# Optimization experiments

Hardware: AMD Instinct MI355X
Metric: run time of the kernel (lower is better)

The kernel has to match this reference:

```python
import jax, jax.numpy as jnp
import numpy as np


def setup_inputs() -> dict:
    key = jax.random.key(0)
    k = jax.random.split(key, 6)
    B, S, d, n = 4, 4096, 1024, 64
    x = jax.random.normal(k[0], (B, S, d), dtype=jnp.float32)
    gate_W = jax.random.normal(k[1], (d, n), dtype=jnp.float32) / np.sqrt(d).astype(np.float32)
    gate_b = jnp.full((n,), 3.0, dtype=jnp.float32)  # nn.init.constant_(gate_proj.bias, 3.0)
    B_W = jax.random.normal(k[2], (d, n), dtype=jnp.float32) / np.sqrt(d).astype(np.float32)
    C_W = jax.random.normal(k[3], (n, d), dtype=jnp.float32) / np.sqrt(n).astype(np.float32)
    out_W = jax.random.normal(k[4], (d, d), dtype=jnp.float32) / np.sqrt(d).astype(np.float32)
    mix_weight = jnp.eye(n, dtype=jnp.float32) + 0.01 * jax.random.normal(k[5], (n, n), dtype=jnp.float32)
    return {"x": x, "gate_W": gate_W, "gate_b": gate_b, "B_W": B_W,
            "C_W": C_W, "out_W": out_W, "mix_weight": mix_weight, "chunk_size": 16}


def _ssm_forward(x, gate_W, gate_b, B_W, C_W, out_W, mix_weight, chunk_size):
    Bb, S, d = x.shape
    n = gate_W.shape[1]
    C = chunk_size
    K = S // C  # seq_len chosen divisible by chunk_size -> F.pad path is a no-op
    # Vectorized per-timestep projections (done once for the whole sequence)
    gates = jax.nn.sigmoid(jnp.einsum('bsd,dn->bsn', x, gate_W) + gate_b)  # a_t in (0,1)
    b_all = jnp.einsum('bsd,dn->bsn', x, B_W)
    a_ch = gates.reshape(Bb, K, C, n).transpose(1, 2, 0, 3)  # (K, C, B, n)
    b_ch = b_all.reshape(Bb, K, C, n).transpose(1, 2, 0, 3)

    def chunk_step(h_prev, ab):
        a_c, b_c = ab  # each (C, B, n)
        def step(h, t):
            a_t, b_t = t
            h = a_t * h + b_t
            return h, h
        h_final, h_stack = jax.lax.scan(step, h_prev, (a_c, b_c))  # h_stack: (C, B, n)
        gate_prod = jnp.prod(a_c, axis=0)  # (B, n) cumulative diag gates
        # T_chunk = mix @ diag(gate_prod): T[b,i,j] = mix[i,j] * gate_prod[b,j]
        T = mix_weight[None, :, :] * gate_prod[:, None, :]
        Th = jnp.einsum('bij,bj->bi', T, h_prev)
        b_chunk = h_final - Th
        h_next = Th + b_chunk  # canonical inter-chunk propagation: T @ h_prev + b_chunk
        return h_next, h_stack

    h0 = jnp.zeros((Bb, n), dtype=x.dtype)
    _, h_all = jax.lax.scan(chunk_step, h0, (a_ch, b_ch))  # (K, C, B, n)
    h_seq = h_all.transpose(2, 0, 1, 3).reshape(Bb, S, n)
    y = jnp.einsum('bsn,nd->bsd', h_seq, C_W)
    out_gate = jax.nn.sigmoid(jnp.einsum('bsd,de->bse', x, out_W))
    return y * out_gate


def reference(x, gate_W, gate_b, B_W, C_W, out_W, mix_weight, chunk_size):
    return _ssm_forward(x, gate_W, gate_b, B_W, C_W, out_W, mix_weight, chunk_size)
```

## Files before the change

kernel.cpp:

```cpp
#include <hip/hip_runtime.h>
#include <stdint.h>

typedef __attribute__((ext_vector_type(8))) short short8;
typedef __attribute__((ext_vector_type(4))) float f32x4;
typedef __attribute__((ext_vector_type(4))) float f4;
typedef __attribute__((ext_vector_type(4))) unsigned short us4;

typedef unsigned short ushort_t;

__device__ __forceinline__ ushort_t f2bf(float f) {
    union { float f; uint32_t u; } c; c.f = f;
    uint32_t u = c.u;
    uint32_t r = u + 0x7fffu + ((u >> 16) & 1u);
    return (ushort_t)(r >> 16);
}
__device__ __forceinline__ float bf2f(ushort_t h) {
    union { uint32_t u; float f; } c; c.u = ((uint32_t)h) << 16;
    return c.f;
}

typedef const __attribute__((address_space(1))) unsigned int as1_uint;
typedef __attribute__((address_space(3))) unsigned int as3_uint;
__device__ __forceinline__ void gload_lds16(const void* g, void* l) {
    __builtin_amdgcn_global_load_lds((as1_uint*)g, (as3_uint*)l, 16, 0, 0);
}

#define SWIDX(r, c) ((r) * 64 + ((c) ^ (((r) & 7) << 3)))

__global__ void prep_weights(const float* __restrict__ gate_W, const float* __restrict__ B_W,
                             const float* __restrict__ C_W, const float* __restrict__ out_W,
                             ushort_t* __restrict__ W1t_hi, ushort_t* __restrict__ W1t_lo,
                             ushort_t* __restrict__ outWt, ushort_t* __restrict__ Ct)
{
    int idx = blockIdx.x * 256 + threadIdx.x;
    int stride = gridDim.x * 256;
    for (int i = idx; i < 1024 * 1024; i += stride) {
        int nn = i >> 10, kk = i & 1023;
        outWt[i] = f2bf(out_W[kk * 1024 + nn]);
    }
    for (int i = idx; i < 128 * 1024; i += stride) {
        int nn = i >> 10, kk = i & 1023;
        float v = (nn < 64) ? gate_W[kk * 64 + nn] : B_W[kk * 64 + (nn - 64)];
        ushort_t h = f2bf(v);
        W1t_hi[i] = h;
        W1t_lo[i] = f2bf(v - bf2f(h));
    }
    for (int i = idx; i < 1024 * 64; i += stride) {
        int nn = i >> 6, kk = i & 63;
        Ct[i] = f2bf(C_W[kk * 1024 + nn]);
    }
}

__global__ __launch_bounds__(256, 2)
void p1_kernel(const float* __restrict__ x,
               const ushort_t* __restrict__ W1t_hi, const ushort_t* __restrict__ W1t_lo,
               ushort_t* __restrict__ x_hi, float* __restrict__ Zpart)
{
    __shared__ ushort_t Ash[128 * 64];
    __shared__ ushort_t Asl[128 * 64];
    __shared__ ushort_t Bsh[64 * 64];

    const int tid = threadIdx.x;
    const int wave = tid >> 6, lane = tid & 63;
    const int wm = wave >> 1, wn = wave & 1;
    const int s0 = blockIdx.x * 64;
    const int kc = blockIdx.y;

    f32x4 acc[4][2];
#pragma unroll
    for (int i = 0; i < 4; i++)
#pragma unroll
        for (int j = 0; j < 2; j++) { f32x4 z = {0.f,0.f,0.f,0.f}; acc[i][j] = z; }

    for (int kt = 0; kt < 8; ++kt) {
        const int k0 = kc * 512 + kt * 64;
#pragma unroll
        for (int p = 0; p < 4; ++p) {
            int c = p * 256 + wave * 64 + lane;
            int row = c >> 3, col = (c & 7) * 8;
            gload_lds16(W1t_hi + (size_t)row * 1024 + k0 + col,
                        &Ash[(p * 256 + wave * 64) * 8]);
            gload_lds16(W1t_lo + (size_t)row * 1024 + k0 + col,
                        &Asl[(p * 256 + wave * 64) * 8]);
        }
#pragma unroll
        for (int p = 0; p < 4; ++p) {
            int f = tid + p * 256;
            int row = f >> 4, col = (f & 15) * 4;
            f4 v = *(const f4*)(x + (size_t)(s0 + row) * 1024 + k0 + col);
            us4 hi;
#pragma unroll
            for (int j = 0; j < 4; j++) hi[j] = f2bf(v[j]);
            *(us4*)&Bsh[row * 64 + col] = hi;
            *(us4*)(x_hi + (size_t)(s0 + row) * 1024 + k0 + col) = hi;
        }
        __syncthreads();
#pragma unroll
        for (int kk = 0; kk < 2; ++kk) {
            const int kb = kk * 32 + (lane >> 4) * 8;
            short8 ah[4], al[4], bh[2];
#pragma unroll
            for (int fm = 0; fm < 4; fm++) {
                int r = wm * 64 + fm * 16 + (lane & 15);
                ah[fm] = *(const short8*)&Ash[r * 64 + kb];
                al[fm] = *(const short8*)&Asl[r * 64 + kb];
            }
#pragma unroll
            for (int fn = 0; fn < 2; fn++) {
                int r = wn * 32 + fn * 16 + (lane & 15);
                bh[fn] = *(const short8*)&Bsh[r * 64 + kb];
            }
#pragma unroll
            for (int fm = 0; fm < 4; fm++)
#pragma unroll
                for (int fn = 0; fn < 2; fn++) {
                    acc[fm][fn] = __builtin_amdgcn_mfma_f32_16x16x32_bf16(ah[fm], bh[fn], acc[fm][fn], 0, 0, 0);
                    acc[fm][fn] = __builtin_amdgcn_mfma_f32_16x16x32_bf16(al[fm], bh[fn], acc[fm][fn], 0, 0, 0);
                }
        }
        __syncthreads();
    }
#pragma unroll
    for (int fm = 0; fm < 4; fm++) {
#pragma unroll
        for (int fn = 0; fn < 2; fn++) {
            int scol = s0 + wn * 32 + fn * 16 + (lane & 15);
            int b = scol >> 12, sb = scol & 4095;
            int nbase = wm * 64 + fm * 16 + ((lane >> 4) << 2);
#pragma unroll
            for (int r = 0; r < 4; r++) {
                Zpart[((size_t)kc * 512 + b * 128 + nbase + r) * 4096 + sb] = acc[fm][fn][r];
            }
        }
    }
}

__global__ __launch_bounds__(256)
void scan_kernel(const float* __restrict__ Zpart, const float* __restrict__ gate_b,
                 ushort_t* __restrict__ hT)
{
    __shared__ float SA[256], SB[256];
    const int bn = blockIdx.x;
    const int t = threadIdx.x;
    const int b = bn >> 6, n = bn & 63;
    const float gb = gate_b[n];
    const float* g0 = Zpart + ((size_t)(b * 128 + n)) * 4096;
    const float* g1 = g0 + (size_t)512 * 4096;
    const float* b0 = Zpart + ((size_t)(b * 128 + 64 + n)) * 4096;
    const float* b1 = b0 + (size_t)512 * 4096;
    const int sb = t * 16;

    float a[16], bb[16];
#pragma unroll
    for (int q = 0; q < 4; q++) {
        f4 vg0 = *(const f4*)(g0 + sb + q * 4);
        f4 vg1 = *(const f4*)(g1 + sb + q * 4);
        f4 vb0 = *(const f4*)(b0 + sb + q * 4);
        f4 vb1 = *(const f4*)(b1 + sb + q * 4);
#pragma unroll
        for (int j = 0; j < 4; j++) {
            a[q * 4 + j] = 1.f / (1.f + __expf(-(vg0[j] + vg1[j] + gb)));
            bb[q * 4 + j] = vb0[j] + vb1[j];
        }
    }
    float A = 1.f, Bv = 0.f;
#pragma unroll
    for (int i = 0; i < 16; i++) { Bv = a[i] * Bv + bb[i]; A *= a[i]; }
    SA[t] = A; SB[t] = Bv;
    __syncthreads();
    for (int off = 1; off < 256; off <<= 1) {
        float a1 = 1.f, b1v = 0.f;
        if (t >= off) { a1 = SA[t - off]; b1v = SB[t - off]; }
        float a2 = SA[t], b2 = SB[t];
        __syncthreads();
        SA[t] = a1 * a2;
        SB[t] = a2 * b1v + b2;
        __syncthreads();
    }
    float h = (t == 0) ? 0.f : SB[t - 1];
    ushort_t ov[16];
#pragma unroll
    for (int i = 0; i < 16; i++) {
        h = a[i] * h + bb[i];
        ov[i] = f2bf(h);
    }
    ushort_t* dst = hT + (size_t)bn * 4096 + sb;
#pragma unroll
    for (int q = 0; q < 4; q++) {
        us4 o; o[0]=ov[q*4]; o[1]=ov[q*4+1]; o[2]=ov[q*4+2]; o[3]=ov[q*4+3];
        *(us4*)(dst + q * 4) = o;
    }
}

__global__ __launch_bounds__(512, 2)
void gemm_out256(const ushort_t* __restrict__ x_hi, const ushort_t* __restrict__ outWt,
                 const ushort_t* __restrict__ hT, const ushort_t* __restrict__ Ct,
                 float* __restrict__ out)
{
    __shared__ ushort_t As[2][256 * 64];
    __shared__ ushort_t Bs[2][256 * 64];

    const int tid = threadIdx.x;
    const int wave = tid >> 6, lane = tid & 63;
    const int wm = wave >> 2;
    const int wn = wave & 3;

    const int flat = blockIdx.x;
    const int swz = (flat & 7) * 32 + (flat >> 3);
    const int m0 = (swz >> 2) * 256;
    const int n0 = (swz & 3) * 256;

    const int lcol0 = (lane >> 4) * 8;
    const int lrow = lane & 15;
    const int lxor = (lrow & 7) << 3;

    const int aOff0 = (wm * 32 + lrow) * 64 + (lcol0 ^ lxor);
    const int aOff1 = (wm * 32 + lrow) * 64 + ((32 + lcol0) ^ lxor);
    const int bOff0 = (wn * 64 + lrow) * 64 + (lcol0 ^ lxor);
    const int bOff1 = (wn * 64 + lrow) * 64 + ((32 + lcol0) ^ lxor);

    const int rl0 = tid >> 3;
    const int col0 = ((tid & 7) ^ (rl0 & 7)) << 3;
    const ushort_t* gB0a = outWt + (size_t)(n0 + rl0) * 1024 + col0;
    const ushort_t* gB0b = gB0a + 64 * 1024;
    const ushort_t* gB1a = outWt + (size_t)(n0 + 128 + rl0) * 1024 + col0;
    const ushort_t* gB1b = gB1a + 64 * 1024;
    const ushort_t* gA0a = x_hi + (size_t)(m0 + rl0) * 1024 + col0;
    const ushort_t* gA0b = gA0a + 64 * 1024;
    const ushort_t* gA1a = x_hi + (size_t)(m0 + 128 + rl0) * 1024 + col0;
    const ushort_t* gA1b = gA1a + 64 * 1024;

    auto STG = [&](const ushort_t*& ga, const ushort_t*& gb, ushort_t* ldsbase) {
        gload_lds16(ga, ldsbase + wave * 512);
        gload_lds16(gb, ldsbase + 4096 + wave * 512);
        ga += 64; gb += 64;
    };

    f32x4 acc[8][4];
#pragma unroll
    for (int i = 0; i < 8; i++)
#pragma unroll
        for (int j = 0; j < 4; j++) { f32x4 z = {0.f,0.f,0.f,0.f}; acc[i][j] = z; }

    STG(gB0a, gB0b, &Bs[0][0]);
    STG(gB1a, gB1b, &Bs[0][8192]);
    STG(gA0a, gA0b, &As[0][0]);
    STG(gA1a, gA1b, &As[0][8192]);
    asm volatile("s_waitcnt vmcnt(2)" ::: "memory");
    __builtin_amdgcn_s_barrier();

#define MFMA_Q(q)                                                                  \
    do {                                                                           \
        __builtin_amdgcn_s_setprio(1);                                             \
        _Pragma("unroll") for (int mm = 0; mm < 2; ++mm)                           \
            _Pragma("unroll") for (int fn = 0; fn < 4; ++fn) {                     \
                acc[2*(q)+mm][fn] = __builtin_amdgcn_mfma_f32_16x16x32_bf16(       \
                    afr[mm][0], bfr[fn][0], acc[2*(q)+mm][fn], 0, 0, 0);           \
                acc[2*(q)+mm][fn] = __builtin_amdgcn_mfma_f32_16x16x32_bf16(       \
                    afr[mm][1], bfr[fn][1], acc[2*(q)+mm][fn], 0, 0, 0);           \
            }                                                                      \
        __builtin_amdgcn_s_setprio(0);                                             \
    } while (0)

    for (int t = 0; t < 16; ++t) {
        const int bc = t & 1;
        const ushort_t* as = &As[bc][0];
        const ushort_t* bs = &Bs[bc][0];
        short8 bfr[4][2], afr[2][2];

#pragma unroll
        for (int fn = 0; fn < 4; ++fn) {
            bfr[fn][0] = *(const short8*)(bs + bOff0 + fn * 1024);
            bfr[fn][1] = *(const short8*)(bs + bOff1 + fn * 1024);
        }
#pragma unroll
        for (int mm = 0; mm < 2; ++mm) {
            afr[mm][0] = *(const short8*)(as + aOff0 + mm * 1024);
            afr[mm][1] = *(const short8*)(as + aOff1 + mm * 1024);
        }
        if (t < 15) STG(gB0a, gB0b, &Bs[bc ^ 1][0]);
        __builtin_amdgcn_s_barrier();
        asm volatile("s_waitcnt lgkmcnt(0)" ::: "memory");
        __builtin_amdgcn_sched_barrier(0);
        MFMA_Q(0);
        __builtin_amdgcn_s_barrier();

#pragma unroll
        for (int mm = 0; mm < 2; ++mm) {
            afr[mm][0] = *(const short8*)(as + aOff0 + 4096 + mm * 1024);
            afr[mm][1] = *(const short8*)(as + aOff1 + 4096 + mm * 1024);
        }
        if (t < 15) {
            STG(gB1a, gB1b, &Bs[bc ^ 1][8192]);
            STG(gA0a, gA0b, &As[bc ^ 1][0]);
        }
        __builtin_amdgcn_s_barrier();
        asm volatile("s_waitcnt lgkmcnt(0)" ::: "memory");
        __builtin_amdgcn_sched_barrier(0);
        MFMA_Q(1);
        if (t < 15) { asm volatile("s_waitcnt vmcnt(6)" ::: "memory"); }
        else        { asm volatile("s_waitcnt vmcnt(0)" ::: "memory"); }
        __builtin_amdgcn_s_barrier();

#pragma unroll
        for (int mm = 0; mm < 2; ++mm) {
            afr[mm][0] = *(const short8*)(as + aOff0 + 2 * 4096 + mm * 1024);
            afr[mm][1] = *(const short8*)(as + aOff1 + 2 * 4096 + mm * 1024);
        }
        if (t < 15) STG(gA1a, gA1b, &As[bc ^ 1][8192]);
        __builtin_amdgcn_s_barrier();
        asm volatile("s_waitcnt lgkmcnt(0)" ::: "memory");
        __builtin_amdgcn_sched_barrier(0);
        MFMA_Q(2);
        __builtin_amdgcn_s_barrier();

#pragma unroll
        for (int mm = 0; mm < 2; ++mm) {
            afr[mm][0] = *(const short8*)(as + aOff0 + 3 * 4096 + mm * 1024);
            afr[mm][1] = *(const short8*)(as + aOff1 + 3 * 4096 + mm * 1024);
        }
        __builtin_amdgcn_s_barrier();
        asm volatile("s_waitcnt lgkmcnt(0)" ::: "memory");
        __builtin_amdgcn_sched_barrier(0);
        MFMA_Q(3);
        if (t < 15) { asm volatile("s_waitcnt vmcnt(2)" ::: "memory"); }
        __builtin_amdgcn_s_barrier();
    }
#undef MFMA_Q

    const int b64 = (m0 >> 12) * 64;
    const int sb0 = m0 & 4095;
#pragma unroll
    for (int p = 0; p < 4; ++p) {
        int c = p * 512 + wave * 64 + lane;
        int row = c >> 3;
        int col = (((c & 7) ^ (row & 7)) << 3);
        gload_lds16(Ct + (size_t)(n0 + row) * 64 + col,
                    &Bs[0][(p * 512 + wave * 64) * 8]);
    }
#pragma unroll
    for (int p = 0; p < 4; ++p) {
        int c = tid + p * 512;
        int kn = c >> 5, mc = c & 31;
        short8 v = *(const short8*)(hT + (size_t)(b64 + kn) * 4096 + sb0 + mc * 8);
#pragma unroll
        for (int j = 0; j < 8; ++j)
            As[0][SWIDX(mc * 8 + j, kn)] = (ushort_t)v[j];
    }
    __syncthreads();

    short8 by[4][2];
#pragma unroll
    for (int fn = 0; fn < 4; fn++)
#pragma unroll
        for (int kk = 0; kk < 2; kk++) {
            int r = wn * 64 + fn * 16 + lrow;
            by[fn][kk] = *(const short8*)&Bs[0][SWIDX(r, kk * 32 + lcol0)];
        }

#pragma unroll
    for (int g = 0; g < 4; g++) {
        f32x4 ty[2][4];
#pragma unroll
        for (int mm = 0; mm < 2; mm++)
#pragma unroll
            for (int fn = 0; fn < 4; fn++) { f32x4 z = {0.f,0.f,0.f,0.f}; ty[mm][fn] = z; }
#pragma unroll
        for (int mm = 0; mm < 2; mm++) {
            int r = g * 64 + wm * 32 + mm * 16 + lrow;
            short8 a0 = *(const short8*)&As[0][SWIDX(r, lcol0)];
            short8 a1 = *(const short8*)&As[0][SWIDX(r, 32 + lcol0)];
#pragma unroll
            for (int fn = 0; fn < 4; fn++) {
                ty[mm][fn] = __builtin_amdgcn_mfma_f32_16x16x32_bf16(a0, by[fn][0], ty[mm][fn], 0, 0, 0);
                ty[mm][fn] = __builtin_amdgcn_mfma_f32_16x16x32_bf16(a1, by[fn][1], ty[mm][fn], 0, 0, 0);
            }
        }
#pragma unroll
        for (int mm = 0; mm < 2; mm++)
#pragma unroll
            for (int fn = 0; fn < 4; fn++) {
                int col = n0 + wn * 64 + fn * 16 + lrow;
                int rbase = m0 + g * 64 + wm * 32 + mm * 16 + ((lane >> 4) << 2);
#pragma unroll
                for (int r = 0; r < 4; r++) {
                    float og = 1.f / (1.f + __expf(-acc[g * 2 + mm][fn][r]));
                    out[(size_t)(rbase + r) * 1024 + col] = ty[mm][fn][r] * og;
                }
            }
    }
}

extern "C" void kernel_launch(void* const* d_in, const int* in_sizes, int n_in,
                              void* d_out, int out_size, void* d_ws, size_t ws_size,
                              hipStream_t stream)
{
    const float* x      = (const float*)d_in[0];
    const float* gate_W = (const float*)d_in[1];
    const float* gate_b = (const float*)d_in[2];
    const float* B_W    = (const float*)d_in[3];
    const float* C_W    = (const float*)d_in[4];
    const float* out_W  = (const float*)d_in[5];
    float* out = (float*)d_out;

    char* ws = (char*)d_ws;
    float*    Zpart  = (float*)(ws + 0);
    ushort_t* hT     = (ushort_t*)(ws + 16777216);
    ushort_t* x_hi   = (ushort_t*)(ws + 18874368);
    ushort_t* W1t_hi = (ushort_t*)(ws + 52428800);
    ushort_t* W1t_lo = (ushort_t*)(ws + 52690944);
    ushort_t* outWt  = (ushort_t*)(ws + 52953088);
    ushort_t* Ct     = (ushort_t*)(ws + 55050240);

    prep_weights<<<512, 256, 0, stream>>>(gate_W, B_W, C_W, out_W,
                                          W1t_hi, W1t_lo, outWt, Ct);

    p1_kernel<<<dim3(256, 2), 256, 0, stream>>>(x, W1t_hi, W1t_lo, x_hi, Zpart);

    scan_kernel<<<256, 256, 0, stream>>>(Zpart, gate_b, hT);

    gemm_out256<<<256, 512, 0, stream>>>(x_hi, outWt, hT, Ct, out);
}
```

Baseline: 91.85 us.

## Double-buffer A fragments in registers and cut barriers in GEMM main loop

New measurement: 83.95 us. 8.6% less time.

```diff
diff --git a/kernel.cpp b/kernel.cpp
--- a/kernel.cpp
+++ b/kernel.cpp
@@ -249,15 +249,22 @@
     asm volatile("s_waitcnt vmcnt(2)" ::: "memory");
     __builtin_amdgcn_s_barrier();
 
-#define MFMA_Q(q)                                                                  \
+    short8 aR0[2][2], aR1[2][2], bfr[4][2];
+#pragma unroll
+    for (int mm = 0; mm < 2; ++mm) {
+        aR0[mm][0] = *(const short8*)&As[0][aOff0 + mm * 1024];
+        aR0[mm][1] = *(const short8*)&As[0][aOff1 + mm * 1024];
+    }
+
+#define MFMA_Q(q, AR)                                                              \
     do {                                                                           \
         __builtin_amdgcn_s_setprio(1);                                             \
         _Pragma("unroll") for (int mm = 0; mm < 2; ++mm)                           \
             _Pragma("unroll") for (int fn = 0; fn < 4; ++fn) {                     \
                 acc[2*(q)+mm][fn] = __builtin_amdgcn_mfma_f32_16x16x32_bf16(       \
-                    afr[mm][0], bfr[fn][0], acc[2*(q)+mm][fn], 0, 0, 0);           \
+                    AR[mm][0], bfr[fn][0], acc[2*(q)+mm][fn], 0, 0, 0);            \
                 acc[2*(q)+mm][fn] = __builtin_amdgcn_mfma_f32_16x16x32_bf16(       \
-                    afr[mm][1], bfr[fn][1], acc[2*(q)+mm][fn], 0, 0, 0);           \
+                    AR[mm][1], bfr[fn][1], acc[2*(q)+mm][fn], 0, 0, 0);            \
             }                                                                      \
         __builtin_amdgcn_s_setprio(0);                                             \
     } while (0)
@@ -266,8 +273,9 @@
         const int bc = t & 1;
         const ushort_t* as = &As[bc][0];
         const ushort_t* bs = &Bs[bc][0];
-        short8 bfr[4][2], afr[2][2];
-
+        const ushort_t* asn = &As[bc ^ 1][0];
+
+        if (t < 15) STG(gB0a, gB0b, &Bs[bc ^ 1][0]);
 #pragma unroll
         for (int fn = 0; fn < 4; ++fn) {
             bfr[fn][0] = *(const short8*)(bs + bOff0 + fn * 1024);
@@ -275,55 +283,54 @@
         }
 #pragma unroll
         for (int mm = 0; mm < 2; ++mm) {
-            afr[mm][0] = *(const short8*)(as + aOff0 + mm * 1024);
-            afr[mm][1] = *(const short8*)(as + aOff1 + mm * 1024);
-        }
-        if (t < 15) STG(gB0a, gB0b, &Bs[bc ^ 1][0]);
+            aR1[mm][0] = *(const short8*)(as + aOff0 + 4096 + mm * 1024);
+            aR1[mm][1] = *(const short8*)(as + aOff1 + 4096 + mm * 1024);
+        }
+        asm volatile("s_waitcnt lgkmcnt(4)" ::: "memory");
+        __builtin_amdgcn_sched_barrier(0);
+        MFMA_Q(0, aR0);
+        if (t < 15) { asm volatile("s_waitcnt vmcnt(2)" ::: "memory"); }
+        else        { asm volatile("s_waitcnt vmcnt(0)" ::: "memory"); }
         __builtin_amdgcn_s_barrier();
-        asm volatile("s_waitcnt lgkmcnt(0)" ::: "memory");
-        __builtin_amdgcn_sched_barrier(0);
-        MFMA_Q(0);
-        __builtin_amdgcn_s_barrier();
-
-#pragma unroll
-        for (int mm = 0; mm < 2; ++mm) {
-            afr[mm][0] = *(const short8*)(as + aOff0 + 4096 + mm * 1024);
-            afr[mm][1] = *(const short8*)(as + aOff1 + 4096 + mm * 1024);
-        }
+
         if (t < 15) {
             STG(gB1a, gB1b, &Bs[bc ^ 1][8192]);
             STG(gA0a, gA0b, &As[bc ^ 1][0]);
         }
+#pragma unroll
+        for (int mm = 0; mm < 2; ++mm) {
+            aR0[mm][0] = *(const short8*)(as + aOff0 + 2 * 4096 + mm * 1024);
+            aR0[mm][1] = *(const short8*)(as + aOff1 + 2 * 4096 + mm * 1024);
+        }
+        asm volatile("s_waitcnt lgkmcnt(4)" ::: "memory");
+        __builtin_amdgcn_sched_barrier(0);
+        MFMA_Q(1, aR1);
         __builtin_amdgcn_s_barrier();
-        asm volatile("s_waitcnt lgkmcnt(0)" ::: "memory");
+
+        if (t < 15) STG(gA1a, gA1b, &As[bc ^ 1][8192]);
+#pragma unroll
+        for (int mm = 0; mm < 2; ++mm) {
+            aR1[mm][0] = *(const short8*)(as + aOff0 + 3 * 4096 + mm * 1024);
+            aR1[mm][1] = *(const short8*)(as + aOff1 + 3 * 4096 + mm * 1024);
+        }
+        asm volatile("s_waitcnt lgkmcnt(4)" ::: "memory");
         __builtin_amdgcn_sched_barrier(0);
-        MFMA_Q(1);
-        if (t < 15) { asm volatile("s_waitcnt vmcnt(6)" ::: "memory"); }
-        else        { asm volatile("s_waitcnt vmcnt(0)" ::: "memory"); }
+        MFMA_Q(2, aR0);
+        if (t < 15) { asm volatile("s_waitcnt vmcnt(2)" ::: "memory"); }
         __builtin_amdgcn_s_barrier();
 
-#pragma unroll
-        for (int mm = 0; mm < 2; ++mm) {
-            afr[mm][0] = *(const short8*)(as + aOff0 + 2 * 4096 + mm * 1024);
-            afr[mm][1] = *(const short8*)(as + aOff1 + 2 * 4096 + mm * 1024);
-        }
-        if (t < 15) STG(gA1a, gA1b, &As[bc ^ 1][8192]);
-        __builtin_amdgcn_s_barrier();
-        asm volatile("s_waitcnt lgkmcnt(0)" ::: "memory");
+        if (t < 15) {
+#pragma unroll
+            for (int mm = 0; mm < 2; ++mm) {
+                aR0[mm][0] = *(const short8*)(asn + aOff0 + mm * 1024);
+                aR0[mm][1] = *(const short8*)(asn + aOff1 + mm * 1024);
+            }
+            asm volatile("s_waitcnt lgkmcnt(4)" ::: "memory");
+        } else {
+            asm volatile("s_waitcnt lgkmcnt(0)" ::: "memory");
+        }
         __builtin_amdgcn_sched_barrier(0);
-        MFMA_Q(2);
-        __builtin_amdgcn_s_barrier();
-
-#pragma unroll
-        for (int mm = 0; mm < 2; ++mm) {
-            afr[mm][0] = *(const short8*)(as + aOff0 + 3 * 4096 + mm * 1024);
-            afr[mm][1] = *(const short8*)(as + aOff1 + 3 * 4096 + mm * 1024);
-        }
-        __builtin_amdgcn_s_barrier();
-        asm volatile("s_waitcnt lgkmcnt(0)" ::: "memory");
-        __builtin_amdgcn_sched_barrier(0);
-        MFMA_Q(3);
-        if (t < 15) { asm volatile("s_waitcnt vmcnt(2)" ::: "memory"); }
+        MFMA_Q(3, aR1);
         __builtin_amdgcn_s_barrier();
     }
 #undef MFMA_Q
@@ -341,7 +348,7 @@
 #pragma unroll
     for (int p = 0; p < 4; ++p) {
         int c = tid + p * 512;
-        int kn = c >> 5, mc = c & 31;
+        int kn = c & 63, mc = c >> 6;
         short8 v = *(const short8*)(hT + (size_t)(b64 + kn) * 4096 + sb0 + mc * 8);
 #pragma unroll
         for (int j = 0; j < 8; ++j)
```
